# Kernel tuning notes

Hardware: AMD Instinct MI355X
Metric: run time of the kernel (lower is better)

The kernel has to match this reference:

```python
import jax, jax.numpy as jnp
import numpy as np

B, T, D, E = 4, 8192, 2048, 64


def setup_inputs() -> dict:
    key = jax.random.key(0)
    k1, k2 = jax.random.split(key)
    x = jax.random.normal(k1, (B, T, D), dtype=jnp.float32)
    kernel_DE = jax.random.normal(k2, (D, E), dtype=jnp.float32) * 0.02
    return {"x": x, "kernel_DE": kernel_DE, "num_experts_per_tok": 8}


def reference(x, kernel_DE, num_experts_per_tok):
    dtype = x.dtype
    # router logits: (B,T,E)
    router_logits_BTE = jnp.einsum("BTD,DE->BTE", x, kernel_DE)
    # gating probs in fp32 for numerical stability
    activated_gating_BTE = jax.nn.softmax(router_logits_BTE.astype(jnp.float32), axis=-1)
    # top-k experts per token
    weights_BTX, selected_experts_BTX = jax.lax.top_k(activated_gating_BTE, num_experts_per_tok)
    # renormalize selected weights via softmax in model dtype (faithful to source)
    normalized_weights_BTX = jax.nn.softmax(weights_BTX.astype(dtype), axis=-1)
    return (normalized_weights_BTX, selected_experts_BTX)
```

## Files before the change

### kernel.cpp

```cpp
#include <hip/hip_runtime.h>
#include <math.h>

#define NTOK  32768
#define DDIM  2048
#define NEXP  64
#define TOPK  8
#define TPW   8
#define WPB   4
#define KC    128
#define GAP_THR  1e-4f
#define LIST_CAP 32000

__global__ void init_ws(int* cnt) { if (threadIdx.x == 0) cnt[0] = 0; }

__global__ __launch_bounds__(256, 3) void router_main(
    const float* __restrict__ x, const float* __restrict__ w,
    float* __restrict__ out, int* __restrict__ cnt, int* __restrict__ list) {
  __shared__ float wlds[KC * NEXP];
  __shared__ float xl[TPW * WPB * KC];

  const int tid  = threadIdx.x;
  const int lane = tid & 63;
  const int wave = tid >> 6;
  const int tok0 = blockIdx.x * (TPW * WPB) + wave * TPW;

  float acc[TPW];
#pragma unroll
  for (int t = 0; t < TPW; ++t) acc[t] = 0.0f;

  for (int c = 0; c < DDIM / KC; ++c) {
    __syncthreads();
    {
      const float4* src = (const float4*)(w + c * (KC * NEXP));
      float4* dst = (float4*)wlds;
#pragma unroll
      for (int i = 0; i < 8; ++i)
        dst[i * 256 + tid] = src[i * 256 + tid];
    }
    {
      float4* xd = (float4*)xl;
#pragma unroll
      for (int i = 0; i < 4; ++i) {
        const int n   = i * 64 + lane;
        const int row = n >> 5;
        const int col = n & 31;
        const float4 v = *(const float4*)(
            x + (size_t)(tok0 + row) * DDIM + c * KC + col * 4);
        xd[wave * 256 + n] = v;
      }
    }
    __syncthreads();

    const float4* xt = (const float4*)xl;
#pragma unroll 2
    for (int d4 = 0; d4 < KC / 4; ++d4) {
      const float w0 = wlds[(d4 * 4 + 0) * NEXP + lane];
      const float w1 = wlds[(d4 * 4 + 1) * NEXP + lane];
      const float w2 = wlds[(d4 * 4 + 2) * NEXP + lane];
      const float w3 = wlds[(d4 * 4 + 3) * NEXP + lane];
#pragma unroll
      for (int t = 0; t < TPW; ++t) {
        const float4 xv = xt[(wave * TPW + t) * (KC / 4) + d4];
        acc[t] = fmaf(xv.x, w0, acc[t]);
        acc[t] = fmaf(xv.y, w1, acc[t]);
        acc[t] = fmaf(xv.z, w2, acc[t]);
        acc[t] = fmaf(xv.w, w3, acc[t]);
      }
    }
  }

  float* out_w = out;
  float* out_i = out + (size_t)NTOK * TOPK;

#pragma unroll 1
  for (int t = 0; t < TPW; ++t) {
    const int tok = tok0 + t;
    const float v = acc[t];

    float m = v;
#pragma unroll
    for (int off = 32; off; off >>= 1) m = fmaxf(m, __shfl_xor(m, off));
    const float ex = __expf(v - m);
    float s = ex;
#pragma unroll
    for (int off = 32; off; off >>= 1) s += __shfl_xor(s, off);
    float pw = ex / s;
    float lw = v;
    int   ii = lane;

    float selp[TOPK + 1];
    float sell[TOPK + 1];
    int   seli[TOPK + 1];
#pragma unroll
    for (int r = 0; r < TOPK + 1; ++r) {
      float bp = pw; float bl = lw; int bi = ii;
#pragma unroll
      for (int off = 32; off; off >>= 1) {
        const float op = __shfl_xor(bp, off);
        const float ol = __shfl_xor(bl, off);
        const int   oi = __shfl_xor(bi, off);
        const bool take = (op > bp) || (op == bp && oi < bi);
        bp = take ? op : bp;
        bl = take ? ol : bl;
        bi = take ? oi : bi;
      }
      selp[r] = bp; sell[r] = bl; seli[r] = bi;
      if (lane == bi) pw = -__builtin_inff();
    }

    bool contested = false;
#pragma unroll
    for (int k = 0; k < TOPK; ++k)
      contested |= (sell[k] - sell[k + 1]) <= GAP_THR;

    const float mm = selp[0];
    float ssum = 0.0f;
#pragma unroll
    for (int k = 0; k < TOPK; ++k) ssum += __expf(selp[k] - mm);
    float myv = selp[0];
    int   myi = seli[0];
#pragma unroll
    for (int k = 1; k < TOPK; ++k)
      if (lane == k) { myv = selp[k]; myi = seli[k]; }
    if (lane < TOPK) {
      out_w[(size_t)tok * TOPK + lane] = __expf(myv - mm) / ssum;
      out_i[(size_t)tok * TOPK + lane] = (float)myi;
    }

    if (contested && lane == 0) {
      const int idx = atomicAdd(cnt, 1);
      if (idx < LIST_CAP) list[idx] = tok;
    }
  }
}

__global__ __launch_bounds__(256, 1) void router_fix(
    const float* __restrict__ x, const float* __restrict__ w,
    float* __restrict__ out, const int* __restrict__ cnt,
    const int* __restrict__ list) {
  const int lane = threadIdx.x & 63;
  const int wave = threadIdx.x >> 6;
  const int gw   = blockIdx.x * 4 + wave;
  const int NW   = gridDim.x * 4;

  int n = cnt[0];
  if (n > LIST_CAP) n = LIST_CAP;

  float* out_w = out;
  float* out_i = out + (size_t)NTOK * TOPK;

  for (int i = gw; i < n; i += NW) {
    const int tok = list[i];
    const float* xr = x + (size_t)tok * DDIM;
    double a0 = 0.0, a1 = 0.0, a2 = 0.0, a3 = 0.0;
#pragma unroll 4
    for (int d4 = 0; d4 < DDIM / 4; ++d4) {
      const float4 xv = *(const float4*)(xr + d4 * 4);
      const int r = d4 * 4;
      a0 = fma((double)xv.x, (double)w[(r + 0) * NEXP + lane], a0);
      a1 = fma((double)xv.y, (double)w[(r + 1) * NEXP + lane], a1);
      a2 = fma((double)xv.z, (double)w[(r + 2) * NEXP + lane], a2);
      a3 = fma((double)xv.w, (double)w[(r + 3) * NEXP + lane], a3);
    }
    const double a = (a0 + a1) + (a2 + a3);

    double dm = a;
#pragma unroll
    for (int off = 32; off; off >>= 1) dm = fmax(dm, __shfl_xor(dm, off));
    const double dex = exp(a - dm);
    double ds = dex;
#pragma unroll
    for (int off = 32; off; off >>= 1) ds += __shfl_xor(ds, off);
    double dpv = dex / ds;

    double dselv[TOPK];
    int    dseli[TOPK];
#pragma unroll
    for (int r = 0; r < TOPK; ++r) {
      double bv = dpv;
      int    bi = lane;
#pragma unroll
      for (int off = 32; off; off >>= 1) {
        const double ov = __shfl_xor(bv, off);
        const int    oi = __shfl_xor(bi, off);
        const bool take = (ov > bv) || (ov == bv && oi < bi);
        bv = take ? ov : bv;
        bi = take ? oi : bi;
      }
      dselv[r] = bv;
      dseli[r] = bi;
      if (lane == bi) dpv = -1.0e300;
    }
    const double dmm = dselv[0];
    double dssum = 0.0;
#pragma unroll
    for (int k = 0; k < TOPK; ++k) dssum += exp(dselv[k] - dmm);
    double myv = dselv[0];
    int    myi = dseli[0];
#pragma unroll
    for (int k = 1; k < TOPK; ++k)
      if (lane == k) { myv = dselv[k]; myi = dseli[k]; }
    if (lane < TOPK) {
      out_w[(size_t)tok * TOPK + lane] = (float)(exp(myv - dmm) / dssum);
      out_i[(size_t)tok * TOPK + lane] = (float)myi;
    }
  }
}

extern "C" void kernel_launch(void* const* d_in, const int* in_sizes, int n_in,
                              void* d_out, int out_size, void* d_ws, size_t ws_size,
                              hipStream_t stream) {
  const float* x = (const float*)d_in[0];
  const float* w = (const float*)d_in[1];
  int* cnt  = (int*)d_ws;
  int* list = (int*)d_ws + 4;

  init_ws<<<dim3(1), dim3(64), 0, stream>>>(cnt);
  router_main<<<dim3(NTOK / (TPW * WPB)), dim3(256), 0, stream>>>(
      x, w, (float*)d_out, cnt, list);
  router_fix<<<dim3(256), dim3(256), 0, stream>>>(
      x, w, (float*)d_out, cnt, list);
}
```

Baseline: 604.9 us.

## Compute router logits with split-bf16 MFMA instead of fp32 FMA

Replaces the LDS-tiled fp32 FMA matmul with bf16 MFMA 16x16x32 instructions. Inputs and weights are split into high and low bf16 parts and combined with three MFMAs to approximate fp32 accuracy. A prep kernel converts the weight matrix into an MFMA fragment layout in the workspace and also zeroes the counter, replacing the init kernel. The split loses a little precision and could add more contested tokens for the fp64 fix-up kernel, and LIST_CAP is reduced.

```diff
diff --git a/kernel.cpp b/kernel.cpp
--- a/kernel.cpp
+++ b/kernel.cpp
@@ -5,77 +5,102 @@
 #define DDIM  2048
 #define NEXP  64
 #define TOPK  8
-#define TPW   8
-#define WPB   4
-#define KC    128
 #define GAP_THR  1e-4f
-#define LIST_CAP 32000
-
-__global__ void init_ws(int* cnt) { if (threadIdx.x == 0) cnt[0] = 0; }
-
-__global__ __launch_bounds__(256, 3) void router_main(
-    const float* __restrict__ x, const float* __restrict__ w,
+#define LIST_CAP 16384
+
+#define WFRAG_OFF  1024
+#define WFRAG_SZ   (64 * 4 * 2048)
+#define LIST_OFF   (WFRAG_OFF + WFRAG_SZ)
+
+typedef __attribute__((ext_vector_type(8))) short s8_t;
+typedef __attribute__((ext_vector_type(4))) float f4_t;
+
+__device__ __forceinline__ unsigned short f2bf(float f) {
+  const unsigned u = __builtin_bit_cast(unsigned, f);
+  const unsigned r = u + 0x7FFFu + ((u >> 16) & 1u);
+  return (unsigned short)(r >> 16);
+}
+
+__global__ void wprep(const float* __restrict__ w, unsigned short* __restrict__ wf,
+                      int* __restrict__ cnt) {
+  if (blockIdx.x == 0 && threadIdx.x == 0) cnt[0] = 0;
+  const int ks   = blockIdx.x;
+  const int eg   = threadIdx.x >> 6;
+  const int lane = threadIdx.x & 63;
+  const int kb   = ks * 32 + ((lane >> 4) << 3);
+  const int e    = (eg << 4) + (lane & 15);
+  s8_t h, l;
+#pragma unroll
+  for (int j = 0; j < 8; ++j) {
+    const float v = w[(size_t)(kb + j) * NEXP + e];
+    const unsigned short hb = f2bf(v);
+    const float hf = __builtin_bit_cast(float, (unsigned)hb << 16);
+    h[j] = (short)hb;
+    l[j] = (short)f2bf(v - hf);
+  }
+  unsigned short* base = wf + (size_t)(ks * 4 + eg) * 1024 + lane * 8;
+  *(s8_t*)(base)       = h;
+  *(s8_t*)(base + 512) = l;
+}
+
+__global__ __launch_bounds__(256, 2) void router_main(
+    const float* __restrict__ x, const unsigned short* __restrict__ wf,
     float* __restrict__ out, int* __restrict__ cnt, int* __restrict__ list) {
-  __shared__ float wlds[KC * NEXP];
-  __shared__ float xl[TPW * WPB * KC];
+  __shared__ float llds[64 * 68];
 
   const int tid  = threadIdx.x;
   const int lane = tid & 63;
   const int wave = tid >> 6;
-  const int tok0 = blockIdx.x * (TPW * WPB) + wave * TPW;
-
-  float acc[TPW];
-#pragma unroll
-  for (int t = 0; t < TPW; ++t) acc[t] = 0.0f;
-
-  for (int c = 0; c < DDIM / KC; ++c) {
-    __syncthreads();
+  const int col  = lane & 15;
+  const int kgrp = lane >> 4;
+  const int wtok = blockIdx.x * 64 + wave * 16;
+
+  f4_t acc[4];
+#pragma unroll
+  for (int eg = 0; eg < 4; ++eg) acc[eg] = (f4_t){0.f, 0.f, 0.f, 0.f};
+
+  const float* xp = x + (size_t)(wtok + col) * DDIM + (kgrp << 3);
+
+#pragma unroll 2
+  for (int ks = 0; ks < DDIM / 32; ++ks) {
+    const float4 v0 = *(const float4*)(xp + ks * 32);
+    const float4 v1 = *(const float4*)(xp + ks * 32 + 4);
+    s8_t ah, al;
     {
-      const float4* src = (const float4*)(w + c * (KC * NEXP));
-      float4* dst = (float4*)wlds;
-#pragma unroll
-      for (int i = 0; i < 8; ++i)
-        dst[i * 256 + tid] = src[i * 256 + tid];
-    }
-    {
-      float4* xd = (float4*)xl;
-#pragma unroll
-      for (int i = 0; i < 4; ++i) {
-        const int n   = i * 64 + lane;
-        const int row = n >> 5;
-        const int col = n & 31;
-        const float4 v = *(const float4*)(
-            x + (size_t)(tok0 + row) * DDIM + c * KC + col * 4);
-        xd[wave * 256 + n] = v;
+      const float xv[8] = {v0.x, v0.y, v0.z, v0.w, v1.x, v1.y, v1.z, v1.w};
+#pragma unroll
+      for (int j = 0; j < 8; ++j) {
+        const unsigned short hb = f2bf(xv[j]);
+        const float hf = __builtin_bit_cast(float, (unsigned)hb << 16);
+        ah[j] = (short)hb;
+        al[j] = (short)f2bf(xv[j] - hf);
       }
     }
-    __syncthreads();
-
-    const float4* xt = (const float4*)xl;
-#pragma unroll 2
-    for (int d4 = 0; d4 < KC / 4; ++d4) {
-      const float w0 = wlds[(d4 * 4 + 0) * NEXP + lane];
-      const float w1 = wlds[(d4 * 4 + 1) * NEXP + lane];
-      const float w2 = wlds[(d4 * 4 + 2) * NEXP + lane];
-      const float w3 = wlds[(d4 * 4 + 3) * NEXP + lane];
-#pragma unroll
-      for (int t = 0; t < TPW; ++t) {
-        const float4 xv = xt[(wave * TPW + t) * (KC / 4) + d4];
-        acc[t] = fmaf(xv.x, w0, acc[t]);
-        acc[t] = fmaf(xv.y, w1, acc[t]);
-        acc[t] = fmaf(xv.z, w2, acc[t]);
-        acc[t] = fmaf(xv.w, w3, acc[t]);
-      }
-    }
-  }
+    const unsigned short* wb = wf + (size_t)ks * 4096 + lane * 8;
+#pragma unroll
+    for (int eg = 0; eg < 4; ++eg) {
+      const s8_t bh = *(const s8_t*)(wb + eg * 1024);
+      const s8_t bl = *(const s8_t*)(wb + eg * 1024 + 512);
+      acc[eg] = __builtin_amdgcn_mfma_f32_16x16x32_bf16(ah, bh, acc[eg], 0, 0, 0);
+      acc[eg] = __builtin_amdgcn_mfma_f32_16x16x32_bf16(al, bh, acc[eg], 0, 0, 0);
+      acc[eg] = __builtin_amdgcn_mfma_f32_16x16x32_bf16(ah, bl, acc[eg], 0, 0, 0);
+    }
+  }
+
+#pragma unroll
+  for (int eg = 0; eg < 4; ++eg)
+#pragma unroll
+    for (int r = 0; r < 4; ++r)
+      llds[(wave * 16 + kgrp * 4 + r) * 68 + eg * 16 + col] = acc[eg][r];
+  __syncthreads();
 
   float* out_w = out;
   float* out_i = out + (size_t)NTOK * TOPK;
 
 #pragma unroll 1
-  for (int t = 0; t < TPW; ++t) {
-    const int tok = tok0 + t;
-    const float v = acc[t];
+  for (int t = 0; t < 16; ++t) {
+    const int tok = wtok + t;
+    const float v = llds[(wave * 16 + t) * 68 + lane];
 
     float m = v;
 #pragma unroll
@@ -212,12 +237,13 @@
                               hipStream_t stream) {
   const float* x = (const float*)d_in[0];
   const float* w = (const float*)d_in[1];
-  int* cnt  = (int*)d_ws;
-  int* list = (int*)d_ws + 4;
-
-  init_ws<<<dim3(1), dim3(64), 0, stream>>>(cnt);
-  router_main<<<dim3(NTOK / (TPW * WPB)), dim3(256), 0, stream>>>(
-      x, w, (float*)d_out, cnt, list);
+  int* cnt = (int*)d_ws;
+  unsigned short* wfrag = (unsigned short*)((char*)d_ws + WFRAG_OFF);
+  int* list = (int*)((char*)d_ws + LIST_OFF);
+
+  wprep<<<dim3(64), dim3(256), 0, stream>>>(w, wfrag, cnt);
+  router_main<<<dim3(NTOK / 64), dim3(256), 0, stream>>>(
+      x, wfrag, (float*)d_out, cnt, list);
   router_fix<<<dim3(256), dim3(256), 0, stream>>>(
       x, w, (float*)d_out, cnt, list);
 }
```

New measurement: 565.4 us. 1.07x faster.
